# Kernel optimization log

Hardware: AMD Instinct MI355X
Metric: run time of the kernel (lower is better)

Reference implementation:

```python
import jax, jax.numpy as jnp
import numpy as np

N = 100000
E = 1600000
D_IN = 128
D_H = 128
N_LAYERS = 3


def setup_inputs() -> dict:
    key = jax.random.key(0)
    ks = jax.random.split(key, 4 + 3 * N_LAYERS)
    x = jax.random.normal(ks[0], (N, D_IN), dtype=jnp.float32)
    edge_index = jax.random.randint(ks[1], (2, E), 0, N, dtype=jnp.int64)
    inp = {"x": x, "edge_index": edge_index}
    d_prev = D_IN
    for i in range(N_LAYERS):
        s = 1.0 / np.sqrt(d_prev)
        inp[f"w_rel{i}"] = jax.random.normal(ks[2 + 3 * i], (D_H, d_prev), dtype=jnp.float32) * s
        inp[f"b_rel{i}"] = jnp.zeros((D_H,), dtype=jnp.float32)
        inp[f"w_root{i}"] = jax.random.normal(ks[3 + 3 * i], (D_H, d_prev), dtype=jnp.float32) * s
        d_prev = D_H
    inp["w_out"] = jax.random.normal(ks[-2], (1, D_H), dtype=jnp.float32) / np.sqrt(D_H)
    inp["b_out"] = jnp.zeros((1,), dtype=jnp.float32)
    return inp


def _graph_conv(x, src, dst, w_rel, b_rel, w_root):
    # PyG GraphConv: out_i = W_rel @ sum_{j->i} x_j + b_rel + W_root @ x_i
    msg = x[src]                                        # [E, d] gather
    aggr = jax.ops.segment_sum(msg, dst, num_segments=N)  # [N, d] scatter-add
    return aggr @ w_rel.T + b_rel + x @ w_root.T


def reference(x, edge_index, w_rel0, b_rel0, w_root0, w_rel1, b_rel1, w_root1,
              w_rel2, b_rel2, w_root2, w_out, b_out):
    src, dst = edge_index[0], edge_index[1]
    params = [(w_rel0, b_rel0, w_root0), (w_rel1, b_rel1, w_root1), (w_rel2, b_rel2, w_root2)]
    h = x
    for w_rel, b_rel, w_root in params:
        h = jax.nn.relu(_graph_conv(h, src, dst, w_rel, b_rel, w_root))
    return h @ w_out.T + b_out  # [N, 1]
```

## Files before the change

### kernel.cpp

```cpp
#include <hip/hip_runtime.h>

constexpr int N_NODES = 100000;
constexpr int N_EDGES = 1600000;
constexpr int CAP = 64;
constexpr int NPB = 128;
constexpr int NBIN = (N_NODES + NPB - 1) / NPB;
constexpr int NGRP = 32;
constexpr int SEGCAP = 128;
constexpr int NBLK_A = 1024;
constexpr int EPB = (N_EDGES + NBLK_A - 1) / NBLK_A;

typedef short short8 __attribute__((ext_vector_type(8)));
typedef float f32x4 __attribute__((ext_vector_type(4)));

__device__ __forceinline__ unsigned short f2bf(float f) {
    unsigned int u = __float_as_uint(f);
    unsigned int r = (u + 0x7fff + ((u >> 16) & 1)) >> 16;
    return (unsigned short)r;
}
__device__ __forceinline__ float bflo(unsigned int u) { return __uint_as_float(u << 16); }
__device__ __forceinline__ float bfhi(unsigned int u) { return __uint_as_float(u & 0xffff0000u); }


__global__ __launch_bounds__(256) void pack_w(const float* __restrict__ wrel,
                                              const float* __restrict__ wroot,
                                              unsigned short* __restrict__ packed) {
    int t = blockIdx.x * 256 + threadIdx.x;
    int j = t & 7, lane = (t >> 3) & 63, ks = (t >> 9) & 7, nt = (t >> 12) & 7;
    int k = ks * 32 + ((lane >> 4) << 3) + j;
    int n = nt * 16 + (lane & 15);
    float v = (k < 128) ? wrel[n * 128 + k] : wroot[n * 128 + (k - 128)];
    packed[t] = f2bf(v);
}

__global__ __launch_bounds__(256) void convert_x(const float* __restrict__ x,
                                                 unsigned short* __restrict__ A) {
    int i = blockIdx.x * 256 + threadIdx.x;
    if (i >= N_NODES * 64) return;
    int node = i >> 6, c2 = (i & 63) * 2;
    float2 v = *(const float2*)&x[(size_t)node * 128 + c2];
    unsigned int out = (unsigned int)f2bf(v.x) | ((unsigned int)f2bf(v.y) << 16);
    *(unsigned int*)&A[(size_t)node * 256 + 128 + c2] = out;
}

__global__ __launch_bounds__(256) void partition_pairs(const int* __restrict__ src,
                                                       const int* __restrict__ dst,
                                                       int* __restrict__ gcnt,
                                                       int* __restrict__ pairs) {
    __shared__ int hist[NBIN];
    __shared__ int bl[NBIN];
    for (int j = threadIdx.x; j < NBIN; j += 256) hist[j] = 0;
    __syncthreads();
    int base = blockIdx.x * EPB;
    int grp = blockIdx.x >> 5;
    int pv[7], pr[7], pb[7];
    bool val[7];
    #pragma unroll
    for (int k = 0; k < 7; ++k) {
        int off = k * 256 + threadIdx.x;
        int e = base + off;
        val[k] = (off < EPB) && (e < N_EDGES);
        pv[k] = pr[k] = pb[k] = 0;
        if (val[k]) {
            int d = __builtin_nontemporal_load(dst + e);
            int s = __builtin_nontemporal_load(src + e);
            pb[k] = d >> 7;
            pv[k] = ((d & 127) << 17) | s;
            pr[k] = atomicAdd(&hist[pb[k]], 1);
        }
    }
    __syncthreads();
    for (int j = threadIdx.x; j < NBIN; j += 256) {
        int h = hist[j];
        bl[j] = h ? atomicAdd(&gcnt[j * NGRP + grp], h) : 0;
    }
    __syncthreads();
    #pragma unroll
    for (int k = 0; k < 7; ++k)
        if (val[k]) {
            int idx = bl[pb[k]] + pr[k];
            if (idx < SEGCAP)
                pairs[((size_t)pb[k] * NGRP + grp) * SEGCAP + idx] = pv[k];
        }
}

__global__ __launch_bounds__(256) void bucket_build(const int* __restrict__ gcnt,
                                                    const int* __restrict__ pairs,
                                                    int* __restrict__ cnt,
                                                    int* __restrict__ bkt) {
    __shared__ int cnt_l[NPB];
    __shared__ int bkt_l[NPB * CAP];
    int j = blockIdx.x;
    for (int t = threadIdx.x; t < NPB; t += 256) cnt_l[t] = 0;
    __syncthreads();
    int wave = threadIdx.x >> 6, lane = threadIdx.x & 63;
    for (int g = wave; g < NGRP; g += 4) {
        int n = gcnt[j * NGRP + g];
        n = (n > SEGCAP) ? SEGCAP : n;
        const int* seg = pairs + ((size_t)j * NGRP + g) * SEGCAP;
        for (int k = lane; k < n; k += 64) {
            int p = __builtin_nontemporal_load(seg + k);
            int dl = p >> 17;
            int s = p & 0x1FFFF;
            int pos = atomicAdd(&cnt_l[dl], 1);
            if (pos < CAP) bkt_l[(dl << 6) + pos] = s;
        }
    }
    __syncthreads();
    int base_node = j * NPB;
    for (int idx = threadIdx.x; idx < NPB * 16; idx += 256) {
        int node = base_node + (idx >> 4);
        if (node < N_NODES)
            ((uint4*)bkt)[(size_t)node * 16 + (idx & 15)] = ((const uint4*)bkt_l)[idx];
    }
    for (int t = threadIdx.x; t < NPB; t += 256) {
        int node = base_node + t;
        if (node < N_NODES) cnt[node] = cnt_l[t];
    }
}

__global__ __launch_bounds__(256) void gather_bucket(const int* __restrict__ cnt_arr,
                                                     const int* __restrict__ bkt,
                                                     unsigned short* __restrict__ A) {
    int wid = (blockIdx.x * 256 + threadIdx.x) >> 6;
    int lane = threadIdx.x & 63;
    if (wid >= N_NODES) return;
    int cnt = cnt_arr[wid];
    cnt = (cnt > CAP) ? CAP : cnt;
    const int* bp = bkt + (wid << 6);
    int g = lane >> 4;
    int ch = lane & 15;
    float acc[8] = {};
    int e = 0;
    for (; e + 8 <= cnt; e += 8) {
        int s0 = bp[e + g];
        int s1 = bp[e + 4 + g];
        uint4 u0 = *(const uint4*)&A[(size_t)s0 * 256 + 128 + ch * 8];
        uint4 u1 = *(const uint4*)&A[(size_t)s1 * 256 + 128 + ch * 8];
        acc[0] += bflo(u0.x); acc[1] += bfhi(u0.x);
        acc[2] += bflo(u0.y); acc[3] += bfhi(u0.y);
        acc[4] += bflo(u0.z); acc[5] += bfhi(u0.z);
        acc[6] += bflo(u0.w); acc[7] += bfhi(u0.w);
        acc[0] += bflo(u1.x); acc[1] += bfhi(u1.x);
        acc[2] += bflo(u1.y); acc[3] += bfhi(u1.y);
        acc[4] += bflo(u1.z); acc[5] += bfhi(u1.z);
        acc[6] += bflo(u1.w); acc[7] += bfhi(u1.w);
    }
    for (; e < cnt; e += 4) {
        int ei = e + g;
        if (ei < cnt) {
            int s0 = bp[ei];
            uint4 u0 = *(const uint4*)&A[(size_t)s0 * 256 + 128 + ch * 8];
            acc[0] += bflo(u0.x); acc[1] += bfhi(u0.x);
            acc[2] += bflo(u0.y); acc[3] += bfhi(u0.y);
            acc[4] += bflo(u0.z); acc[5] += bfhi(u0.z);
            acc[6] += bflo(u0.w); acc[7] += bfhi(u0.w);
        }
    }
    #pragma unroll
    for (int j = 0; j < 8; ++j) {
        acc[j] += __shfl_xor(acc[j], 16);
        acc[j] += __shfl_xor(acc[j], 32);
    }
    if (g == 0) {
        uint4 o;
        o.x = (unsigned int)f2bf(acc[0]) | ((unsigned int)f2bf(acc[1]) << 16);
        o.y = (unsigned int)f2bf(acc[2]) | ((unsigned int)f2bf(acc[3]) << 16);
        o.z = (unsigned int)f2bf(acc[4]) | ((unsigned int)f2bf(acc[5]) << 16);
        o.w = (unsigned int)f2bf(acc[6]) | ((unsigned int)f2bf(acc[7]) << 16);
        *(uint4*)&A[(size_t)wid * 256 + ch * 8] = o;
    }
}

template <bool LAST>
__global__ __launch_bounds__(256) void mfma_transform(unsigned short* __restrict__ A,
                                                      const unsigned short* __restrict__ packedW,
                                                      const float* __restrict__ brel,
                                                      const float* __restrict__ w_out,
                                                      const float* __restrict__ b_out,
                                                      float* __restrict__ outF) {
    __shared__ unsigned short sW[32768];
    {
        const uint4* g = (const uint4*)packedW;
        uint4* s = (uint4*)sW;
        for (int i = threadIdx.x; i < 4096; i += 256) s[i] = g[i];
    }
    __syncthreads();
    int wave = threadIdx.x >> 6, lane = threadIdx.x & 63;
    int l15 = lane & 15, lhi = lane >> 4;
    int brow = blockIdx.x * 256 + wave * 64;
    float bias[8], wo[8];
    #pragma unroll
    for (int nt = 0; nt < 8; ++nt) {
        bias[nt] = brel[nt * 16 + l15];
        if (LAST) wo[nt] = w_out[nt * 16 + l15];
    }
    float bout = LAST ? b_out[0] : 0.f;

    for (int rtp = 0; rtp < 2; ++rtp) {
        int r0 = brow + rtp * 32;
        short8 a[2][8];
        #pragma unroll
        for (int rt = 0; rt < 2; ++rt) {
            int row = r0 + rt * 16 + l15;
            if (row >= N_NODES) row = N_NODES - 1;
            const unsigned short* ap = &A[(size_t)row * 256 + lhi * 8];
            #pragma unroll
            for (int ks = 0; ks < 8; ++ks) a[rt][ks] = *(const short8*)(ap + ks * 32);
        }
        f32x4 acc[2][8] = {};
        #pragma unroll
        for (int nt = 0; nt < 8; ++nt) {
            #pragma unroll
            for (int ks = 0; ks < 8; ++ks) {
                short8 b = *(const short8*)&sW[(size_t)((nt * 8 + ks) * 64 + lane) * 8];
                acc[0][nt] = __builtin_amdgcn_mfma_f32_16x16x32_bf16(a[0][ks], b, acc[0][nt], 0, 0, 0);
                acc[1][nt] = __builtin_amdgcn_mfma_f32_16x16x32_bf16(a[1][ks], b, acc[1][nt], 0, 0, 0);
            }
        }
        #pragma unroll
        for (int rt = 0; rt < 2; ++rt) {
            if (LAST) {
                #pragma unroll
                for (int rg = 0; rg < 4; ++rg) {
                    float p = 0.f;
                    #pragma unroll
                    for (int nt = 0; nt < 8; ++nt)
                        p += fmaxf(acc[rt][nt][rg] + bias[nt], 0.f) * wo[nt];
                    p += __shfl_xor(p, 1);
                    p += __shfl_xor(p, 2);
                    p += __shfl_xor(p, 4);
                    p += __shfl_xor(p, 8);
                    int row = r0 + rt * 16 + lhi * 4 + rg;
                    if (l15 == 0 && row < N_NODES) outF[row] = p + bout;
                }
            } else {
                #pragma unroll
                for (int nt = 0; nt < 8; ++nt) {
                    #pragma unroll
                    for (int rg = 0; rg < 4; ++rg) {
                        int row = r0 + rt * 16 + lhi * 4 + rg;
                        if (row < N_NODES) {
                            float v = fmaxf(acc[rt][nt][rg] + bias[nt], 0.f);
                            A[(size_t)row * 256 + 128 + nt * 16 + l15] = f2bf(v);
                        }
                    }
                }
            }
        }
    }
}

extern "C" void kernel_launch(void* const* d_in, const int* in_sizes, int n_in,
                              void* d_out, int out_size, void* d_ws, size_t ws_size,
                              hipStream_t stream) {
    const float* x      = (const float*)d_in[0];
    const int*   edge   = (const int*)d_in[1];
    const int*   src    = edge;
    const int*   dst    = edge + N_EDGES;
    const float* w_rel[3]  = {(const float*)d_in[2], (const float*)d_in[5], (const float*)d_in[8]};
    const float* b_rel[3]  = {(const float*)d_in[3], (const float*)d_in[6], (const float*)d_in[9]};
    const float* w_root[3] = {(const float*)d_in[4], (const float*)d_in[7], (const float*)d_in[10]};
    const float* w_out  = (const float*)d_in[11];
    const float* b_out  = (const float*)d_in[12];

    unsigned short* A  = (unsigned short*)d_ws;
    unsigned short* pW = A + (size_t)N_NODES * 256;
    int* cnt   = (int*)(pW + 3 * 32768);
    int* bkt   = cnt + N_NODES;
    int* gcnt  = bkt + (size_t)N_NODES * CAP;
    int* pairs = gcnt + NBIN * NGRP;

    for (int i = 0; i < 3; ++i)
        pack_w<<<128, 256, 0, stream>>>(w_rel[i], w_root[i], pW + (size_t)i * 32768);
    convert_x<<<(N_NODES * 64 + 255) / 256, 256, 0, stream>>>(x, A);

    hipMemsetAsync(gcnt, 0, NBIN * NGRP * sizeof(int), stream);
    partition_pairs<<<NBLK_A, 256, 0, stream>>>(src, dst, gcnt, pairs);
    bucket_build<<<NBIN, 256, 0, stream>>>(gcnt, pairs, cnt, bkt);

    const int gblocks = (N_NODES * 64 + 255) / 256;
    const int xblocks = (N_NODES + 255) / 256;

    gather_bucket<<<gblocks, 256, 0, stream>>>(cnt, bkt, A);
    mfma_transform<false><<<xblocks, 256, 0, stream>>>(A, pW + 0 * 32768, b_rel[0],
                                                       nullptr, nullptr, nullptr);
    gather_bucket<<<gblocks, 256, 0, stream>>>(cnt, bkt, A);
    mfma_transform<false><<<xblocks, 256, 0, stream>>>(A, pW + 1 * 32768, b_rel[1],
                                                       nullptr, nullptr, nullptr);
    gather_bucket<<<gblocks, 256, 0, stream>>>(cnt, bkt, A);
    mfma_transform<true><<<xblocks, 256, 0, stream>>>(A, pW + 2 * 32768, b_rel[2],
                                                      w_out, b_out, (float*)d_out);
}
```

Before: 358.1 us.

## Fuse neighbor gather with MFMA transform per layer using ping-pong feature buffers

```diff
diff --git a/kernel.cpp b/kernel.cpp
--- a/kernel.cpp
+++ b/kernel.cpp
@@ -21,7 +21,6 @@
 __device__ __forceinline__ float bflo(unsigned int u) { return __uint_as_float(u << 16); }
 __device__ __forceinline__ float bfhi(unsigned int u) { return __uint_as_float(u & 0xffff0000u); }
 
-
 __global__ __launch_bounds__(256) void pack_w(const float* __restrict__ wrel,
                                               const float* __restrict__ wroot,
                                               unsigned short* __restrict__ packed) {
@@ -34,13 +33,13 @@
 }
 
 __global__ __launch_bounds__(256) void convert_x(const float* __restrict__ x,
-                                                 unsigned short* __restrict__ A) {
+                                                 unsigned short* __restrict__ h) {
     int i = blockIdx.x * 256 + threadIdx.x;
     if (i >= N_NODES * 64) return;
     int node = i >> 6, c2 = (i & 63) * 2;
     float2 v = *(const float2*)&x[(size_t)node * 128 + c2];
     unsigned int out = (unsigned int)f2bf(v.x) | ((unsigned int)f2bf(v.y) << 16);
-    *(unsigned int*)&A[(size_t)node * 256 + 128 + c2] = out;
+    *(unsigned int*)&h[(size_t)node * 128 + c2] = out;
 }
 
 __global__ __launch_bounds__(256) void partition_pairs(const int* __restrict__ src,
@@ -119,76 +118,71 @@
     }
 }
 
-__global__ __launch_bounds__(256) void gather_bucket(const int* __restrict__ cnt_arr,
-                                                     const int* __restrict__ bkt,
-                                                     unsigned short* __restrict__ A) {
-    int wid = (blockIdx.x * 256 + threadIdx.x) >> 6;
-    int lane = threadIdx.x & 63;
-    if (wid >= N_NODES) return;
-    int cnt = cnt_arr[wid];
-    cnt = (cnt > CAP) ? CAP : cnt;
-    const int* bp = bkt + (wid << 6);
-    int g = lane >> 4;
-    int ch = lane & 15;
-    float acc[8] = {};
-    int e = 0;
-    for (; e + 8 <= cnt; e += 8) {
-        int s0 = bp[e + g];
-        int s1 = bp[e + 4 + g];
-        uint4 u0 = *(const uint4*)&A[(size_t)s0 * 256 + 128 + ch * 8];
-        uint4 u1 = *(const uint4*)&A[(size_t)s1 * 256 + 128 + ch * 8];
-        acc[0] += bflo(u0.x); acc[1] += bfhi(u0.x);
-        acc[2] += bflo(u0.y); acc[3] += bfhi(u0.y);
-        acc[4] += bflo(u0.z); acc[5] += bfhi(u0.z);
-        acc[6] += bflo(u0.w); acc[7] += bfhi(u0.w);
-        acc[0] += bflo(u1.x); acc[1] += bfhi(u1.x);
-        acc[2] += bflo(u1.y); acc[3] += bfhi(u1.y);
-        acc[4] += bflo(u1.z); acc[5] += bfhi(u1.z);
-        acc[6] += bflo(u1.w); acc[7] += bfhi(u1.w);
-    }
-    for (; e < cnt; e += 4) {
-        int ei = e + g;
-        if (ei < cnt) {
-            int s0 = bp[ei];
-            uint4 u0 = *(const uint4*)&A[(size_t)s0 * 256 + 128 + ch * 8];
+template <bool LAST>
+__global__ __launch_bounds__(256) void fused_layer(const int* __restrict__ cnt_arr,
+                                                   const int* __restrict__ bkt,
+                                                   const unsigned short* __restrict__ h_in,
+                                                   const unsigned short* __restrict__ packedW,
+                                                   const float* __restrict__ brel,
+                                                   const float* __restrict__ w_out,
+                                                   const float* __restrict__ b_out,
+                                                   unsigned short* __restrict__ h_out,
+                                                   float* __restrict__ outF) {
+    __shared__ uint4 sA[4][16][16];
+    int wave = threadIdx.x >> 6, lane = threadIdx.x & 63;
+    int l15 = lane & 15, lhi = lane >> 4;
+    int wrow0 = blockIdx.x * 64 + wave * 16;
+
+    int g = lhi;
+    int ch = l15;
+    for (int r = 0; r < 16; ++r) {
+        int node = wrow0 + r;
+        if (node >= N_NODES) break;
+        int cnt = cnt_arr[node];
+        cnt = (cnt > CAP) ? CAP : cnt;
+        const int* bp = bkt + (node << 6);
+        float acc[8] = {};
+        int e = 0;
+        for (; e + 8 <= cnt; e += 8) {
+            int s0 = bp[e + g];
+            int s1 = bp[e + 4 + g];
+            uint4 u0 = *(const uint4*)&h_in[(size_t)s0 * 128 + ch * 8];
+            uint4 u1 = *(const uint4*)&h_in[(size_t)s1 * 128 + ch * 8];
             acc[0] += bflo(u0.x); acc[1] += bfhi(u0.x);
             acc[2] += bflo(u0.y); acc[3] += bfhi(u0.y);
             acc[4] += bflo(u0.z); acc[5] += bfhi(u0.z);
             acc[6] += bflo(u0.w); acc[7] += bfhi(u0.w);
-        }
-    }
-    #pragma unroll
-    for (int j = 0; j < 8; ++j) {
-        acc[j] += __shfl_xor(acc[j], 16);
-        acc[j] += __shfl_xor(acc[j], 32);
-    }
-    if (g == 0) {
-        uint4 o;
-        o.x = (unsigned int)f2bf(acc[0]) | ((unsigned int)f2bf(acc[1]) << 16);
-        o.y = (unsigned int)f2bf(acc[2]) | ((unsigned int)f2bf(acc[3]) << 16);
-        o.z = (unsigned int)f2bf(acc[4]) | ((unsigned int)f2bf(acc[5]) << 16);
-        o.w = (unsigned int)f2bf(acc[6]) | ((unsigned int)f2bf(acc[7]) << 16);
-        *(uint4*)&A[(size_t)wid * 256 + ch * 8] = o;
-    }
-}
-
-template <bool LAST>
-__global__ __launch_bounds__(256) void mfma_transform(unsigned short* __restrict__ A,
-                                                      const unsigned short* __restrict__ packedW,
-                                                      const float* __restrict__ brel,
-                                                      const float* __restrict__ w_out,
-                                                      const float* __restrict__ b_out,
-                                                      float* __restrict__ outF) {
-    __shared__ unsigned short sW[32768];
-    {
-        const uint4* g = (const uint4*)packedW;
-        uint4* s = (uint4*)sW;
-        for (int i = threadIdx.x; i < 4096; i += 256) s[i] = g[i];
-    }
-    __syncthreads();
-    int wave = threadIdx.x >> 6, lane = threadIdx.x & 63;
-    int l15 = lane & 15, lhi = lane >> 4;
-    int brow = blockIdx.x * 256 + wave * 64;
+            acc[0] += bflo(u1.x); acc[1] += bfhi(u1.x);
+            acc[2] += bflo(u1.y); acc[3] += bfhi(u1.y);
+            acc[4] += bflo(u1.z); acc[5] += bfhi(u1.z);
+            acc[6] += bflo(u1.w); acc[7] += bfhi(u1.w);
+        }
+        for (; e < cnt; e += 4) {
+            int ei = e + g;
+            if (ei < cnt) {
+                int s0 = bp[ei];
+                uint4 u0 = *(const uint4*)&h_in[(size_t)s0 * 128 + ch * 8];
+                acc[0] += bflo(u0.x); acc[1] += bfhi(u0.x);
+                acc[2] += bflo(u0.y); acc[3] += bfhi(u0.y);
+                acc[4] += bflo(u0.z); acc[5] += bfhi(u0.z);
+                acc[6] += bflo(u0.w); acc[7] += bfhi(u0.w);
+            }
+        }
+        #pragma unroll
+        for (int j = 0; j < 8; ++j) {
+            acc[j] += __shfl_xor(acc[j], 16);
+            acc[j] += __shfl_xor(acc[j], 32);
+        }
+        if (g == 0) {
+            uint4 o;
+            o.x = (unsigned int)f2bf(acc[0]) | ((unsigned int)f2bf(acc[1]) << 16);
+            o.y = (unsigned int)f2bf(acc[2]) | ((unsigned int)f2bf(acc[3]) << 16);
+            o.z = (unsigned int)f2bf(acc[4]) | ((unsigned int)f2bf(acc[5]) << 16);
+            o.w = (unsigned int)f2bf(acc[6]) | ((unsigned int)f2bf(acc[7]) << 16);
+            sA[wave][r][ch ^ r] = o;
+        }
+    }
+
     float bias[8], wo[8];
     #pragma unroll
     for (int nt = 0; nt < 8; ++nt) {
@@ -197,54 +191,51 @@
     }
     float bout = LAST ? b_out[0] : 0.f;
 
-    for (int rtp = 0; rtp < 2; ++rtp) {
-        int r0 = brow + rtp * 32;
-        short8 a[2][8];
-        #pragma unroll
-        for (int rt = 0; rt < 2; ++rt) {
-            int row = r0 + rt * 16 + l15;
-            if (row >= N_NODES) row = N_NODES - 1;
-            const unsigned short* ap = &A[(size_t)row * 256 + lhi * 8];
+    short8 a[8];
+    #pragma unroll
+    for (int ks = 0; ks < 4; ++ks) {
+        uint4 t = sA[wave][l15][(ks * 4 + lhi) ^ l15];
+        a[ks] = *(short8*)&t;
+    }
+    int hrow = wrow0 + l15;
+    if (hrow >= N_NODES) hrow = N_NODES - 1;
+    #pragma unroll
+    for (int ks = 4; ks < 8; ++ks)
+        a[ks] = *(const short8*)&h_in[(size_t)hrow * 128 + (ks - 4) * 32 + lhi * 8];
+
+    f32x4 acc2[8] = {};
+    #pragma unroll
+    for (int nt = 0; nt < 8; ++nt) {
+        #pragma unroll
+        for (int ks = 0; ks < 8; ++ks) {
+            short8 b = *(const short8*)&packedW[(size_t)((nt * 8 + ks) * 64 + lane) * 8];
+            acc2[nt] = __builtin_amdgcn_mfma_f32_16x16x32_bf16(a[ks], b, acc2[nt], 0, 0, 0);
+        }
+    }
+
+    if (LAST) {
+        #pragma unroll
+        for (int rg = 0; rg < 4; ++rg) {
+            float p = 0.f;
             #pragma unroll
-            for (int ks = 0; ks < 8; ++ks) a[rt][ks] = *(const short8*)(ap + ks * 32);
-        }
-        f32x4 acc[2][8] = {};
+            for (int nt = 0; nt < 8; ++nt)
+                p += fmaxf(acc2[nt][rg] + bias[nt], 0.f) * wo[nt];
+            p += __shfl_xor(p, 1);
+            p += __shfl_xor(p, 2);
+            p += __shfl_xor(p, 4);
+            p += __shfl_xor(p, 8);
+            int row = wrow0 + lhi * 4 + rg;
+            if (l15 == 0 && row < N_NODES) outF[row] = p + bout;
+        }
+    } else {
         #pragma unroll
         for (int nt = 0; nt < 8; ++nt) {
             #pragma unroll
-            for (int ks = 0; ks < 8; ++ks) {
-                short8 b = *(const short8*)&sW[(size_t)((nt * 8 + ks) * 64 + lane) * 8];
-                acc[0][nt] = __builtin_amdgcn_mfma_f32_16x16x32_bf16(a[0][ks], b, acc[0][nt], 0, 0, 0);
-                acc[1][nt] = __builtin_amdgcn_mfma_f32_16x16x32_bf16(a[1][ks], b, acc[1][nt], 0, 0, 0);
-            }
-        }
-        #pragma unroll
-        for (int rt = 0; rt < 2; ++rt) {
-            if (LAST) {
-                #pragma unroll
-                for (int rg = 0; rg < 4; ++rg) {
-                    float p = 0.f;
-                    #pragma unroll
-                    for (int nt = 0; nt < 8; ++nt)
-                        p += fmaxf(acc[rt][nt][rg] + bias[nt], 0.f) * wo[nt];
-                    p += __shfl_xor(p, 1);
-                    p += __shfl_xor(p, 2);
-                    p += __shfl_xor(p, 4);
-                    p += __shfl_xor(p, 8);
-                    int row = r0 + rt * 16 + lhi * 4 + rg;
-                    if (l15 == 0 && row < N_NODES) outF[row] = p + bout;
-                }
-            } else {
-                #pragma unroll
-                for (int nt = 0; nt < 8; ++nt) {
-                    #pragma unroll
-                    for (int rg = 0; rg < 4; ++rg) {
-                        int row = r0 + rt * 16 + lhi * 4 + rg;
-                        if (row < N_NODES) {
-                            float v = fmaxf(acc[rt][nt][rg] + bias[nt], 0.f);
-                            A[(size_t)row * 256 + 128 + nt * 16 + l15] = f2bf(v);
-                        }
-                    }
+            for (int rg = 0; rg < 4; ++rg) {
+                int row = wrow0 + lhi * 4 + rg;
+                if (row < N_NODES) {
+                    float v = fmaxf(acc2[nt][rg] + bias[nt], 0.f);
+                    h_out[(size_t)row * 128 + nt * 16 + l15] = f2bf(v);
                 }
             }
         }
@@ -264,8 +255,9 @@
     const float* w_out  = (const float*)d_in[11];
     const float* b_out  = (const float*)d_in[12];
 
-    unsigned short* A  = (unsigned short*)d_ws;
-    unsigned short* pW = A + (size_t)N_NODES * 256;
+    unsigned short* hA = (unsigned short*)d_ws;
+    unsigned short* hB = hA + (size_t)N_NODES * 128;
+    unsigned short* pW = hB + (size_t)N_NODES * 128;
     int* cnt   = (int*)(pW + 3 * 32768);
     int* bkt   = cnt + N_NODES;
     int* gcnt  = bkt + (size_t)N_NODES * CAP;
@@ -273,22 +265,18 @@
 
     for (int i = 0; i < 3; ++i)
         pack_w<<<128, 256, 0, stream>>>(w_rel[i], w_root[i], pW + (size_t)i * 32768);
-    convert_x<<<(N_NODES * 64 + 255) / 256, 256, 0, stream>>>(x, A);
+    convert_x<<<(N_NODES * 64 + 255) / 256, 256, 0, stream>>>(x, hA);
 
     hipMemsetAsync(gcnt, 0, NBIN * NGRP * sizeof(int), stream);
     partition_pairs<<<NBLK_A, 256, 0, stream>>>(src, dst, gcnt, pairs);
     bucket_build<<<NBIN, 256, 0, stream>>>(gcnt, pairs, cnt, bkt);
 
-    const int gblocks = (N_NODES * 64 + 255) / 256;
-    const int xblocks = (N_NODES + 255) / 256;
-
-    gather_bucket<<<gblocks, 256, 0, stream>>>(cnt, bkt, A);
-    mfma_transform<false><<<xblocks, 256, 0, stream>>>(A, pW + 0 * 32768, b_rel[0],
-                                                       nullptr, nullptr, nullptr);
-    gather_bucket<<<gblocks, 256, 0, stream>>>(cnt, bkt, A);
-    mfma_transform<false><<<xblocks, 256, 0, stream>>>(A, pW + 1 * 32768, b_rel[1],
-                                                       nullptr, nullptr, nullptr);
-    gather_bucket<<<gblocks, 256, 0, stream>>>(cnt, bkt, A);
-    mfma_transform<true><<<xblocks, 256, 0, stream>>>(A, pW + 2 * 32768, b_rel[2],
-                                                      w_out, b_out, (float*)d_out);
-}
+    const int fblocks = (N_NODES + 63) / 64;
+
+    fused_layer<false><<<fblocks, 256, 0, stream>>>(cnt, bkt, hA, pW + 0 * 32768, b_rel[0],
+                                                    nullptr, nullptr, hB, nullptr);
+    fused_layer<false><<<fblocks, 256, 0, stream>>>(cnt, bkt, hB, pW + 1 * 32768, b_rel[1],
+                                                    nullptr, nullptr, hA, nullptr);
+    fused_layer<true><<<fblocks, 256, 0, stream>>>(cnt, bkt, hA, pW + 2 * 32768, b_rel[2],
+                                                   w_out, b_out, nullptr, (float*)d_out);
+}
```

Result: slower. 448.8 us (+25.3%).
